# Optimization experiments

Hardware: AMD Instinct MI355X
Metric: run time of the kernel (lower is better)

## Reference

```python
import jax, jax.numpy as jnp
import numpy as np

D_MODEL = 1024
NUM_HEADS = 16
D_K = D_MODEL // NUM_HEADS


def setup_inputs() -> dict:
    key = jax.random.key(0)
    k_x, k_q, k_k, k_v, k_o = jax.random.split(key, 5)
    s = 1.0 / np.sqrt(D_MODEL)
    return {
        "x": jax.random.normal(k_x, (2, 2048, D_MODEL), dtype=jnp.float32),
        "W_q": jax.random.normal(k_q, (D_MODEL, D_MODEL), dtype=jnp.float32) * s,
        "W_k": jax.random.normal(k_k, (D_MODEL, D_MODEL), dtype=jnp.float32) * s,
        "W_v": jax.random.normal(k_v, (D_MODEL, D_MODEL), dtype=jnp.float32) * s,
        "W_o": jax.random.normal(k_o, (D_MODEL, D_MODEL), dtype=jnp.float32) * s,
    }


def reference(x, W_q, W_k, W_v, W_o):
    B, S, D = x.shape
    H, dk = NUM_HEADS, D_K
    # nn.Linear(y) = y @ W.T ; weights stored as (out, in)
    def proj(W):
        return (x @ W.T).reshape(B, S, H, dk).transpose(0, 2, 1, 3)  # (B,H,S,dk)
    Q, K, V = proj(W_q), proj(W_k), proj(W_v)
    scores = jnp.einsum("bhqd,bhkd->bhqk", Q, K) / np.sqrt(dk)  # (B,H,S,S)
    attn = jax.nn.softmax(scores, axis=-1)
    out = jnp.einsum("bhqk,bhkd->bhqd", attn, V)  # (B,H,S,dk)
    out = out.transpose(0, 2, 1, 3).reshape(B, S, D)
    return out @ W_o.T
```

## Files before the change

kernel.cpp:

```cpp
#include <hip/hip_runtime.h>
#include <hip/hip_bf16.h>

#define SEQ 2048
#define DM  1024
#define NH  16
#define DK  64
#define MROWS 4096

typedef __attribute__((ext_vector_type(8))) short short8;
typedef __attribute__((ext_vector_type(4))) short short4v;
typedef __attribute__((ext_vector_type(4))) float float4v;

typedef const __attribute__((address_space(1))) unsigned gu32;
typedef __attribute__((address_space(3))) unsigned lu32;

__device__ __forceinline__ void gl2lds16(const void* g, void* l) {
  __builtin_amdgcn_global_load_lds((gu32*)g, (lu32*)l, 16, 0, 0);
}

__device__ __forceinline__ short f2bf(float f) {
  union { float f; unsigned u; } v; v.f = f;
  unsigned r = v.u + 0x7fffu + ((v.u >> 16) & 1u);
  return (short)(r >> 16);
}
__device__ __forceinline__ short f2bfu(float f) {
  union { float f; unsigned u; } v; v.f = f;
  return (short)((v.u + 0x8000u) >> 16);
}

__global__ __launch_bounds__(256) void cvt_kernel(
    const float* __restrict__ in, short* __restrict__ out) {
  int i = blockIdx.x * 256 + threadIdx.x;
  float4v f = ((const float4v*)in)[i];
  short4v s;
#pragma unroll
  for (int j = 0; j < 4; ++j) s[j] = f2bf(f[j]);
  ((short4v*)out)[i] = s;
}

__global__ __launch_bounds__(256) void cvt4_kernel(
    const float* __restrict__ a, const float* __restrict__ b,
    const float* __restrict__ c, const float* __restrict__ d,
    short* __restrict__ out) {
  const float* srcs[4] = {a, b, c, d};
  const float* s = srcs[blockIdx.y];
  int i = blockIdx.x * 256 + threadIdx.x;
  float4v f = ((const float4v*)s)[i];
  short4v sv;
#pragma unroll
  for (int j = 0; j < 4; ++j) sv[j] = f2bf(f[j]);
  ((short4v*)(out + (size_t)blockIdx.y * DM * DM))[i] = sv;
}

template<typename TC>
__global__ __launch_bounds__(512) void gemm_bt_kernel(
    const short* __restrict__ A, const short* __restrict__ Bw0,
    TC* __restrict__ C0, int M, int N, int K, size_t strB, size_t strC)
{
  __shared__ __align__(16) short Al[2][128 * 72];
  __shared__ __align__(16) short Bl[2][128 * 72];
  const short* Bw = Bw0 + (size_t)blockIdx.z * strB;
  TC* C = C0 + (size_t)blockIdx.z * strC;

  const int tid  = threadIdx.x;
  const int lane = tid & 63, wave = tid >> 6;
  const int l16  = lane & 15, quad = lane >> 4;
  const int wm   = (wave >> 2) * 64, wn = (wave & 3) * 32;
  const int cm   = blockIdx.y * 128, cn = blockIdx.x * 128;

  const int r0 = tid >> 3,        c0 = (tid & 7) * 8;
  const int r1 = (512 + tid) >> 3, c1 = c0;

  float4v acc[4][2];
#pragma unroll
  for (int i = 0; i < 4; ++i)
#pragma unroll
    for (int j = 0; j < 2; ++j)
#pragma unroll
      for (int r = 0; r < 4; ++r) acc[i][j][r] = 0.f;

  const short* ag = A  + (size_t)cm * K;
  const short* bg = Bw + (size_t)cn * K;

  short8 ra0, ra1, rb0, rb1;
  auto loadG = [&](int k0) {
    ra0 = *(const short8*)(ag + (size_t)r0 * K + k0 + c0);
    ra1 = *(const short8*)(ag + (size_t)r1 * K + k0 + c1);
    rb0 = *(const short8*)(bg + (size_t)r0 * K + k0 + c0);
    rb1 = *(const short8*)(bg + (size_t)r1 * K + k0 + c1);
  };
  auto writeL = [&](int buf) {
    *(short8*)&Al[buf][r0 * 72 + c0] = ra0;
    *(short8*)&Al[buf][r1 * 72 + c1] = ra1;
    *(short8*)&Bl[buf][r0 * 72 + c0] = rb0;
    *(short8*)&Bl[buf][r1 * 72 + c1] = rb1;
  };
  auto compute = [&](int buf) {
#pragma unroll
    for (int ks = 0; ks < 2; ++ks) {
      short8 af[4], bf[2];
#pragma unroll
      for (int mi = 0; mi < 4; ++mi)
        af[mi] = *(const short8*)&Al[buf][(wm + mi*16 + l16) * 72 + ks*32 + quad*8];
#pragma unroll
      for (int ni = 0; ni < 2; ++ni)
        bf[ni] = *(const short8*)&Bl[buf][(wn + ni*16 + l16) * 72 + ks*32 + quad*8];
#pragma unroll
      for (int mi = 0; mi < 4; ++mi)
#pragma unroll
        for (int ni = 0; ni < 2; ++ni)
          acc[mi][ni] = __builtin_amdgcn_mfma_f32_16x16x32_bf16(
              af[mi], bf[ni], acc[mi][ni], 0, 0, 0);
    }
  };

  loadG(0);
  writeL(0);
  __syncthreads();
  int cur = 0;
  for (int k0 = 0; k0 < K; k0 += 64) {
    bool nxt = (k0 + 64 < K);
    if (nxt) loadG(k0 + 64);
    compute(cur);
    if (nxt) writeL(cur ^ 1);
    __syncthreads();
    cur ^= 1;
  }

#pragma unroll
  for (int mi = 0; mi < 4; ++mi)
#pragma unroll
    for (int ni = 0; ni < 2; ++ni)
#pragma unroll
      for (int r = 0; r < 4; ++r) {
        int m = cm + wm + mi*16 + quad*4 + r;
        int n = cn + wn + ni*16 + l16;
        float v = acc[mi][ni][r];
        if constexpr (sizeof(TC) == 2) C[(size_t)m * N + n] = f2bf(v);
        else                           C[(size_t)m * N + n] = v;
      }
}

__global__ __launch_bounds__(512) void flash_kernel(
    const short* __restrict__ Q, const short* __restrict__ Kb,
    const short* __restrict__ Vb, short* __restrict__ AO)
{
  __shared__ __align__(16) short Kl[2][64 * 64];
  __shared__ __align__(16) short Vt[2][64 * 72];
  __shared__ __align__(16) short Pl[8][16 * 72];
  const int tid  = threadIdx.x;
  const int lane = tid & 63, wave = tid >> 6;
  const int l16  = lane & 15, quad = lane >> 4;
  const int q0   = blockIdx.x * 128;
  const int hc   = blockIdx.y * DK;
  const size_t base = (size_t)blockIdx.z * SEQ;

  short8 qf[2];
#pragma unroll
  for (int ks = 0; ks < 2; ++ks)
    qf[ks] = *(const short8*)(Q + (base + q0 + wave*16 + l16) * DM
                              + hc + ks*32 + quad*8);

  float4v O[4];
  float lsum[4];
#pragma unroll
  for (int d = 0; d < 4; ++d)
#pragma unroll
    for (int r = 0; r < 4; ++r) O[d][r] = 0.f;
#pragma unroll
  for (int r = 0; r < 4; ++r) lsum[r] = 0.f;

  const float sc = 0.18033688011112042f;

  auto stageK = [&](int buf, int kb) {
    int row = tid >> 3, col = (tid & 7) * 8;
    gl2lds16(Kb + (base + kb*64 + row) * DM + hc + col, &Kl[buf][wave * 512]);
  };
  auto loadV = [&](int kb) -> short8 {
    return *(const short8*)(Vb + (base + kb*64 + lane) * DM + hc + wave*8);
  };
  auto writeV = [&](int buf, short8 v8) {
#pragma unroll
    for (int j = 0; j < 8; ++j) Vt[buf][(wave*8 + j) * 72 + lane] = v8[j];
  };

  {
    short8 v0 = loadV(0);
    stageK(0, 0);
    writeV(0, v0);
  }
  __syncthreads();

  int cur = 0;
  for (int kb = 0; kb < SEQ / 64; ++kb) {
    bool has_next = (kb + 1 < SEQ / 64);
    short8 vnext;
    if (has_next) { vnext = loadV(kb + 1); stageK(cur ^ 1, kb + 1); }

    float4v s[4];
#pragma unroll
    for (int nt = 0; nt < 4; ++nt)
#pragma unroll
      for (int r = 0; r < 4; ++r) s[nt][r] = 0.f;
#pragma unroll
    for (int ks = 0; ks < 2; ++ks) {
#pragma unroll
      for (int nt = 0; nt < 4; ++nt) {
        short8 kf = *(const short8*)&Kl[cur][(nt*16 + l16) * 64 + ks*32 + quad*8];
        s[nt] = __builtin_amdgcn_mfma_f32_16x16x32_bf16(qf[ks], kf, s[nt], 0, 0, 0);
      }
    }
#pragma unroll
    for (int r = 0; r < 4; ++r) {
      float p0 = exp2f(s[0][r] * sc), p1 = exp2f(s[1][r] * sc);
      float p2 = exp2f(s[2][r] * sc), p3 = exp2f(s[3][r] * sc);
      lsum[r] += (p0 + p1) + (p2 + p3);
      int pr = (quad*4 + r) * 72;
      Pl[wave][pr + l16]      = f2bfu(p0);
      Pl[wave][pr + 16 + l16] = f2bfu(p1);
      Pl[wave][pr + 32 + l16] = f2bfu(p2);
      Pl[wave][pr + 48 + l16] = f2bfu(p3);
    }
#pragma unroll
    for (int ks = 0; ks < 2; ++ks) {
      short8 pf = *(const short8*)&Pl[wave][l16 * 72 + ks*32 + quad*8];
#pragma unroll
      for (int d = 0; d < 4; ++d) {
        short8 vfd = *(const short8*)&Vt[cur][(d*16 + l16) * 72 + ks*32 + quad*8];
        O[d] = __builtin_amdgcn_mfma_f32_16x16x32_bf16(pf, vfd, O[d], 0, 0, 0);
      }
    }
    if (has_next) writeV(cur ^ 1, vnext);
    __syncthreads();
    cur ^= 1;
  }

#pragma unroll
  for (int r = 0; r < 4; ++r) {
    float l = lsum[r];
    l += __shfl_xor(l, 1, 64);
    l += __shfl_xor(l, 2, 64);
    l += __shfl_xor(l, 4, 64);
    l += __shfl_xor(l, 8, 64);
    float inv = 1.f / l;
    int m = q0 + wave*16 + quad*4 + r;
#pragma unroll
    for (int d = 0; d < 4; ++d)
      AO[(base + m) * DM + hc + d*16 + l16] = f2bf(O[d][r] * inv);
  }
}

extern "C" void kernel_launch(void* const* d_in, const int* in_sizes, int n_in,
                              void* d_out, int out_size, void* d_ws, size_t ws_size,
                              hipStream_t stream) {
  (void)in_sizes; (void)n_in; (void)out_size; (void)ws_size;
  const float* x  = (const float*)d_in[0];
  const float* Wq = (const float*)d_in[1];
  const float* Wk = (const float*)d_in[2];
  const float* Wv = (const float*)d_in[3];
  const float* Wo = (const float*)d_in[4];
  float* out = (float*)d_out;

  const size_t NX = (size_t)MROWS * DM;
  const size_t NW = (size_t)DM * DM;
  short* xb  = (short*)d_ws;
  short* Wqb = xb  + NX;
  short* Qb  = Wqb + 4 * NW;
  short* AO  = Qb  + 3 * NX;

  cvt_kernel<<<dim3(NX / 4 / 256), 256, 0, stream>>>(x, xb);
  cvt4_kernel<<<dim3(NW / 4 / 256, 4), 256, 0, stream>>>(Wq, Wk, Wv, Wo, Wqb);

  gemm_bt_kernel<short><<<dim3(DM / 128, MROWS / 128, 3), 512, 0, stream>>>(
      xb, Wqb, Qb, MROWS, DM, DM, NW, NX);

  flash_kernel<<<dim3(SEQ / 128, NH, 2), 512, 0, stream>>>(
      Qb, Qb + NX, Qb + 2 * NX, AO);

  gemm_bt_kernel<float><<<dim3(DM / 128, MROWS / 128, 1), 512, 0, stream>>>(
      AO, Wqb + 3 * NW, out, MROWS, DM, DM, 0, 0);
}
```

Measured before the change: 222.8 us.

## Emit transposed V from projection GEMM and enlarge per-wave tiles in GEMM and flash

The QKV projection GEMM now writes V already transposed through an LDS staging tile, so flash attention loads V^T rows directly and no longer scatters V into LDS. Both kernels drop to 256 threads. Each GEMM wave now computes a 64x64 tile, and each flash wave handles 32 query rows, reusing K and V fragments across two query tiles. K is now staged with regular loads into padded LDS instead of global_load_lds. The aim is fewer LDS transposes and more MFMA work per fragment load, at the cost of higher register pressure and lower occupancy.

```diff
diff --git a/kernel.cpp b/kernel.cpp
--- a/kernel.cpp
+++ b/kernel.cpp
@@ -10,13 +10,6 @@
 typedef __attribute__((ext_vector_type(8))) short short8;
 typedef __attribute__((ext_vector_type(4))) short short4v;
 typedef __attribute__((ext_vector_type(4))) float float4v;
-
-typedef const __attribute__((address_space(1))) unsigned gu32;
-typedef __attribute__((address_space(3))) unsigned lu32;
-
-__device__ __forceinline__ void gl2lds16(const void* g, void* l) {
-  __builtin_amdgcn_global_load_lds((gu32*)g, (lu32*)l, 16, 0, 0);
-}
 
 __device__ __forceinline__ short f2bf(float f) {
   union { float f; unsigned u; } v; v.f = f;
@@ -53,9 +46,10 @@
 }
 
 template<typename TC>
-__global__ __launch_bounds__(512) void gemm_bt_kernel(
+__global__ __launch_bounds__(256) void gemm_bt_kernel(
     const short* __restrict__ A, const short* __restrict__ Bw0,
-    TC* __restrict__ C0, int M, int N, int K, size_t strB, size_t strC)
+    TC* __restrict__ C0, int M, int N, int K, size_t strB, size_t strC,
+    short* __restrict__ vtOut)
 {
   __shared__ __align__(16) short Al[2][128 * 72];
   __shared__ __align__(16) short Bl[2][128 * 72];
@@ -65,52 +59,55 @@
   const int tid  = threadIdx.x;
   const int lane = tid & 63, wave = tid >> 6;
   const int l16  = lane & 15, quad = lane >> 4;
-  const int wm   = (wave >> 2) * 64, wn = (wave & 3) * 32;
+  const int wm   = (wave >> 1) * 64, wn = (wave & 1) * 64;
   const int cm   = blockIdx.y * 128, cn = blockIdx.x * 128;
 
-  const int r0 = tid >> 3,        c0 = (tid & 7) * 8;
-  const int r1 = (512 + tid) >> 3, c1 = c0;
-
-  float4v acc[4][2];
+  float4v acc[4][4];
 #pragma unroll
   for (int i = 0; i < 4; ++i)
 #pragma unroll
-    for (int j = 0; j < 2; ++j)
+    for (int j = 0; j < 4; ++j)
 #pragma unroll
       for (int r = 0; r < 4; ++r) acc[i][j][r] = 0.f;
 
   const short* ag = A  + (size_t)cm * K;
   const short* bg = Bw + (size_t)cn * K;
-
-  short8 ra0, ra1, rb0, rb1;
+  int rw[4];
+#pragma unroll
+  for (int it = 0; it < 4; ++it) rw[it] = (it * 256 + tid) >> 3;
+  const int cl = (tid & 7) * 8;
+
+  short8 ra[4], rb[4];
   auto loadG = [&](int k0) {
-    ra0 = *(const short8*)(ag + (size_t)r0 * K + k0 + c0);
-    ra1 = *(const short8*)(ag + (size_t)r1 * K + k0 + c1);
-    rb0 = *(const short8*)(bg + (size_t)r0 * K + k0 + c0);
-    rb1 = *(const short8*)(bg + (size_t)r1 * K + k0 + c1);
+#pragma unroll
+    for (int it = 0; it < 4; ++it) {
+      ra[it] = *(const short8*)(ag + (size_t)rw[it] * K + k0 + cl);
+      rb[it] = *(const short8*)(bg + (size_t)rw[it] * K + k0 + cl);
+    }
   };
   auto writeL = [&](int buf) {
-    *(short8*)&Al[buf][r0 * 72 + c0] = ra0;
-    *(short8*)&Al[buf][r1 * 72 + c1] = ra1;
-    *(short8*)&Bl[buf][r0 * 72 + c0] = rb0;
-    *(short8*)&Bl[buf][r1 * 72 + c1] = rb1;
+#pragma unroll
+    for (int it = 0; it < 4; ++it) {
+      *(short8*)&Al[buf][rw[it] * 72 + cl] = ra[it];
+      *(short8*)&Bl[buf][rw[it] * 72 + cl] = rb[it];
+    }
   };
   auto compute = [&](int buf) {
 #pragma unroll
     for (int ks = 0; ks < 2; ++ks) {
-      short8 af[4], bf[2];
+      short8 af[4], bfr[4];
 #pragma unroll
       for (int mi = 0; mi < 4; ++mi)
         af[mi] = *(const short8*)&Al[buf][(wm + mi*16 + l16) * 72 + ks*32 + quad*8];
 #pragma unroll
-      for (int ni = 0; ni < 2; ++ni)
-        bf[ni] = *(const short8*)&Bl[buf][(wn + ni*16 + l16) * 72 + ks*32 + quad*8];
+      for (int ni = 0; ni < 4; ++ni)
+        bfr[ni] = *(const short8*)&Bl[buf][(wn + ni*16 + l16) * 72 + ks*32 + quad*8];
 #pragma unroll
       for (int mi = 0; mi < 4; ++mi)
 #pragma unroll
-        for (int ni = 0; ni < 2; ++ni)
+        for (int ni = 0; ni < 4; ++ni)
           acc[mi][ni] = __builtin_amdgcn_mfma_f32_16x16x32_bf16(
-              af[mi], bf[ni], acc[mi][ni], 0, 0, 0);
+              af[mi], bfr[ni], acc[mi][ni], 0, 0, 0);
     }
   };
 
@@ -127,27 +124,48 @@
     cur ^= 1;
   }
 
-#pragma unroll
-  for (int mi = 0; mi < 4; ++mi)
-#pragma unroll
-    for (int ni = 0; ni < 2; ++ni)
-#pragma unroll
-      for (int r = 0; r < 4; ++r) {
-        int m = cm + wm + mi*16 + quad*4 + r;
-        int n = cn + wn + ni*16 + l16;
-        float v = acc[mi][ni][r];
-        if constexpr (sizeof(TC) == 2) C[(size_t)m * N + n] = f2bf(v);
-        else                           C[(size_t)m * N + n] = v;
-      }
-}
-
-__global__ __launch_bounds__(512) void flash_kernel(
-    const short* __restrict__ Q, const short* __restrict__ Kb,
-    const short* __restrict__ Vb, short* __restrict__ AO)
+  if (vtOut != nullptr && blockIdx.z == 2) {
+    short* T = &Al[0][0];
+#pragma unroll
+    for (int mi = 0; mi < 4; ++mi)
+#pragma unroll
+      for (int ni = 0; ni < 4; ++ni)
+#pragma unroll
+        for (int r = 0; r < 4; ++r)
+          T[(wn + ni*16 + l16) * 136 + wm + mi*16 + quad*4 + r] =
+              f2bf(acc[mi][ni][r]);
+    __syncthreads();
+    const int nrow = tid >> 1, mo = (tid & 1) * 64;
+    const int b = cm >> 11;
+    const int s0 = (cm & (SEQ - 1)) + mo;
+    short* vt = vtOut + ((size_t)b * DM + cn + nrow) * SEQ + s0;
+#pragma unroll
+    for (int j = 0; j < 8; ++j)
+      *(short8*)(vt + j * 8) = *(const short8*)&T[nrow * 136 + mo + j * 8];
+  } else {
+#pragma unroll
+    for (int mi = 0; mi < 4; ++mi)
+#pragma unroll
+      for (int ni = 0; ni < 4; ++ni)
+#pragma unroll
+        for (int r = 0; r < 4; ++r) {
+          int m = cm + wm + mi*16 + quad*4 + r;
+          int n = cn + wn + ni*16 + l16;
+          float v = acc[mi][ni][r];
+          if constexpr (sizeof(TC) == 2) C[(size_t)m * N + n] = f2bf(v);
+          else                           C[(size_t)m * N + n] = v;
+        }
+  }
+}
+
+__global__ __launch_bounds__(256) void flash_kernel(
+    const short* __restrict__ Q, const short* __restrict__ Kg,
+    const short* __restrict__ VTg, short* __restrict__ AO)
 {
-  __shared__ __align__(16) short Kl[2][64 * 64];
+  __shared__ __align__(16) short Kl[2][64 * 72];
   __shared__ __align__(16) short Vt[2][64 * 72];
-  __shared__ __align__(16) short Pl[8][16 * 72];
+  __shared__ __align__(16) short Pl[4][32 * 72];
+  __shared__ float lsumL[4][32];
   const int tid  = threadIdx.x;
   const int lane = tid & 63, wave = tid >> 6;
   const int l16  = lane & 15, quad = lane >> 4;
@@ -155,98 +173,121 @@
   const int hc   = blockIdx.y * DK;
   const size_t base = (size_t)blockIdx.z * SEQ;
 
-  short8 qf[2];
-#pragma unroll
-  for (int ks = 0; ks < 2; ++ks)
-    qf[ks] = *(const short8*)(Q + (base + q0 + wave*16 + l16) * DM
-                              + hc + ks*32 + quad*8);
-
-  float4v O[4];
-  float lsum[4];
-#pragma unroll
-  for (int d = 0; d < 4; ++d)
-#pragma unroll
-    for (int r = 0; r < 4; ++r) O[d][r] = 0.f;
-#pragma unroll
-  for (int r = 0; r < 4; ++r) lsum[r] = 0.f;
+  short8 qfr[2][2];
+#pragma unroll
+  for (int qf = 0; qf < 2; ++qf)
+#pragma unroll
+    for (int ks = 0; ks < 2; ++ks)
+      qfr[qf][ks] = *(const short8*)(Q + (base + q0 + wave*32 + qf*16 + l16) * DM
+                                     + hc + ks*32 + quad*8);
+
+  float4v O[2][4];
+  float lsum[2] = {0.f, 0.f};
+#pragma unroll
+  for (int mt = 0; mt < 2; ++mt)
+#pragma unroll
+    for (int nt = 0; nt < 4; ++nt)
+#pragma unroll
+      for (int r = 0; r < 4; ++r) O[mt][nt][r] = 0.f;
 
   const float sc = 0.18033688011112042f;
 
-  auto stageK = [&](int buf, int kb) {
-    int row = tid >> 3, col = (tid & 7) * 8;
-    gl2lds16(Kb + (base + kb*64 + row) * DM + hc + col, &Kl[buf][wave * 512]);
-  };
-  auto loadV = [&](int kb) -> short8 {
-    return *(const short8*)(Vb + (base + kb*64 + lane) * DM + hc + wave*8);
-  };
-  auto writeV = [&](int buf, short8 v8) {
-#pragma unroll
-    for (int j = 0; j < 8; ++j) Vt[buf][(wave*8 + j) * 72 + lane] = v8[j];
-  };
-
-  {
-    short8 v0 = loadV(0);
-    stageK(0, 0);
-    writeV(0, v0);
-  }
+  const int r0 = tid >> 3, r1 = (256 + tid) >> 3;
+  const int c0 = (tid & 7) * 8;
+  const short* vtb = VTg + ((size_t)blockIdx.z * DM + hc) * SEQ;
+
+  short8 ka0, ka1, va0, va1;
+  auto loadKV = [&](int kb) {
+    ka0 = *(const short8*)(Kg + (base + kb*64 + r0) * DM + hc + c0);
+    ka1 = *(const short8*)(Kg + (base + kb*64 + r1) * DM + hc + c0);
+    va0 = *(const short8*)(vtb + (size_t)r0 * SEQ + kb*64 + c0);
+    va1 = *(const short8*)(vtb + (size_t)r1 * SEQ + kb*64 + c0);
+  };
+  auto writeKV = [&](int buf) {
+    *(short8*)&Kl[buf][r0 * 72 + c0] = ka0;
+    *(short8*)&Kl[buf][r1 * 72 + c0] = ka1;
+    *(short8*)&Vt[buf][r0 * 72 + c0] = va0;
+    *(short8*)&Vt[buf][r1 * 72 + c0] = va1;
+  };
+
+  loadKV(0);
+  writeKV(0);
   __syncthreads();
 
   int cur = 0;
   for (int kb = 0; kb < SEQ / 64; ++kb) {
-    bool has_next = (kb + 1 < SEQ / 64);
-    short8 vnext;
-    if (has_next) { vnext = loadV(kb + 1); stageK(cur ^ 1, kb + 1); }
-
-    float4v s[4];
-#pragma unroll
-    for (int nt = 0; nt < 4; ++nt)
-#pragma unroll
-      for (int r = 0; r < 4; ++r) s[nt][r] = 0.f;
+    bool nxt = (kb + 1 < SEQ / 64);
+    if (nxt) loadKV(kb + 1);
+
+    float4v s[4][2];
+#pragma unroll
+    for (int kf = 0; kf < 4; ++kf)
+#pragma unroll
+      for (int qf = 0; qf < 2; ++qf)
+#pragma unroll
+        for (int r = 0; r < 4; ++r) s[kf][qf][r] = 0.f;
 #pragma unroll
     for (int ks = 0; ks < 2; ++ks) {
 #pragma unroll
+      for (int kf = 0; kf < 4; ++kf) {
+        short8 kfr = *(const short8*)&Kl[cur][(kf*16 + l16) * 72 + ks*32 + quad*8];
+#pragma unroll
+        for (int qf = 0; qf < 2; ++qf)
+          s[kf][qf] = __builtin_amdgcn_mfma_f32_16x16x32_bf16(
+              kfr, qfr[qf][ks], s[kf][qf], 0, 0, 0);
+      }
+    }
+#pragma unroll
+    for (int kf = 0; kf < 4; ++kf)
+#pragma unroll
+      for (int qf = 0; qf < 2; ++qf) {
+        float p0 = exp2f(s[kf][qf][0] * sc), p1 = exp2f(s[kf][qf][1] * sc);
+        float p2 = exp2f(s[kf][qf][2] * sc), p3 = exp2f(s[kf][qf][3] * sc);
+        lsum[qf] += (p0 + p1) + (p2 + p3);
+        short4v pk;
+        pk[0] = f2bfu(p0); pk[1] = f2bfu(p1); pk[2] = f2bfu(p2); pk[3] = f2bfu(p3);
+        *(short4v*)&Pl[wave][(qf*16 + l16) * 72 + kf*16 + quad*4] = pk;
+      }
+#pragma unroll
+    for (int ks = 0; ks < 2; ++ks) {
+      short8 pf[2];
+#pragma unroll
+      for (int mt = 0; mt < 2; ++mt)
+        pf[mt] = *(const short8*)&Pl[wave][(mt*16 + l16) * 72 + ks*32 + quad*8];
+#pragma unroll
       for (int nt = 0; nt < 4; ++nt) {
-        short8 kf = *(const short8*)&Kl[cur][(nt*16 + l16) * 64 + ks*32 + quad*8];
-        s[nt] = __builtin_amdgcn_mfma_f32_16x16x32_bf16(qf[ks], kf, s[nt], 0, 0, 0);
+        short8 vf = *(const short8*)&Vt[cur][(nt*16 + l16) * 72 + ks*32 + quad*8];
+#pragma unroll
+        for (int mt = 0; mt < 2; ++mt)
+          O[mt][nt] = __builtin_amdgcn_mfma_f32_16x16x32_bf16(
+              pf[mt], vf, O[mt][nt], 0, 0, 0);
       }
     }
-#pragma unroll
-    for (int r = 0; r < 4; ++r) {
-      float p0 = exp2f(s[0][r] * sc), p1 = exp2f(s[1][r] * sc);
-      float p2 = exp2f(s[2][r] * sc), p3 = exp2f(s[3][r] * sc);
-      lsum[r] += (p0 + p1) + (p2 + p3);
-      int pr = (quad*4 + r) * 72;
-      Pl[wave][pr + l16]      = f2bfu(p0);
-      Pl[wave][pr + 16 + l16] = f2bfu(p1);
-      Pl[wave][pr + 32 + l16] = f2bfu(p2);
-      Pl[wave][pr + 48 + l16] = f2bfu(p3);
-    }
-#pragma unroll
-    for (int ks = 0; ks < 2; ++ks) {
-      short8 pf = *(const short8*)&Pl[wave][l16 * 72 + ks*32 + quad*8];
-#pragma unroll
-      for (int d = 0; d < 4; ++d) {
-        short8 vfd = *(const short8*)&Vt[cur][(d*16 + l16) * 72 + ks*32 + quad*8];
-        O[d] = __builtin_amdgcn_mfma_f32_16x16x32_bf16(pf, vfd, O[d], 0, 0, 0);
-      }
-    }
-    if (has_next) writeV(cur ^ 1, vnext);
+    if (nxt) writeKV(cur ^ 1);
     __syncthreads();
     cur ^= 1;
   }
 
 #pragma unroll
-  for (int r = 0; r < 4; ++r) {
-    float l = lsum[r];
-    l += __shfl_xor(l, 1, 64);
-    l += __shfl_xor(l, 2, 64);
-    l += __shfl_xor(l, 4, 64);
-    l += __shfl_xor(l, 8, 64);
-    float inv = 1.f / l;
-    int m = q0 + wave*16 + quad*4 + r;
-#pragma unroll
-    for (int d = 0; d < 4; ++d)
-      AO[(base + m) * DM + hc + d*16 + l16] = f2bf(O[d][r] * inv);
+  for (int qf = 0; qf < 2; ++qf) {
+    float l = lsum[qf];
+    l += __shfl_xor(l, 16, 64);
+    l += __shfl_xor(l, 32, 64);
+    lsumL[wave][qf*16 + l16] = l;
+  }
+#pragma unroll
+  for (int mt = 0; mt < 2; ++mt) {
+    float inv[4];
+#pragma unroll
+    for (int r = 0; r < 4; ++r)
+      inv[r] = 1.f / lsumL[wave][mt*16 + quad*4 + r];
+#pragma unroll
+    for (int nt = 0; nt < 4; ++nt)
+#pragma unroll
+      for (int r = 0; r < 4; ++r) {
+        int m = q0 + wave*32 + mt*16 + quad*4 + r;
+        AO[(base + m) * DM + hc + nt*16 + l16] = f2bf(O[mt][nt][r] * inv[r]);
+      }
   }
 }
 
@@ -266,17 +307,18 @@
   short* xb  = (short*)d_ws;
   short* Wqb = xb  + NX;
   short* Qb  = Wqb + 4 * NW;
-  short* AO  = Qb  + 3 * NX;
+  short* Kb  = Qb  + NX;
+  short* AO  = Kb  + NX;
+  short* VTb = AO  + NX;
 
   cvt_kernel<<<dim3(NX / 4 / 256), 256, 0, stream>>>(x, xb);
   cvt4_kernel<<<dim3(NW / 4 / 256, 4), 256, 0, stream>>>(Wq, Wk, Wv, Wo, Wqb);
 
-  gemm_bt_kernel<short><<<dim3(DM / 128, MROWS / 128, 3), 512, 0, stream>>>(
-      xb, Wqb, Qb, MROWS, DM, DM, NW, NX);
-
-  flash_kernel<<<dim3(SEQ / 128, NH, 2), 512, 0, stream>>>(
-      Qb, Qb + NX, Qb + 2 * NX, AO);
-
-  gemm_bt_kernel<float><<<dim3(DM / 128, MROWS / 128, 1), 512, 0, stream>>>(
-      AO, Wqb + 3 * NW, out, MROWS, DM, DM, 0, 0);
-}
+  gemm_bt_kernel<short><<<dim3(DM / 128, MROWS / 128, 3), 256, 0, stream>>>(
+      xb, Wqb, Qb, MROWS, DM, DM, NW, NX, VTb);
+
+  flash_kernel<<<dim3(SEQ / 128, NH, 2), 256, 0, stream>>>(Qb, Kb, VTb, AO);
+
+  gemm_bt_kernel<float><<<dim3(DM / 128, MROWS / 128, 1), 256, 0, stream>>>(
+      AO, Wqb + 3 * NW, out, MROWS, DM, DM, 0, 0, nullptr);
+}
```

New measurement: 214.7 us. 1.04x faster.
